# Kernel optimization log

Measured on AMD Instinct MI355X. Metric: run time of the kernel, lower is better.

The kernel has to match this reference:

```python
import jax, jax.numpy as jnp
import numpy as np

D_MODEL = 1024
D_STATE = 64
D_CONV = 4
EXPAND = 2
HEADDIM = 64
NGROUPS = 1
D_INNER = EXPAND * D_MODEL          # 2048 (= d_ssm)
NHEADS = D_INNER // HEADDIM         # 32
CONV_DIM = D_INNER + 2 * NGROUPS * D_STATE      # 2176
D_IN_PROJ = 2 * D_INNER + 2 * NGROUPS * D_STATE + NHEADS  # 4256
BATCH, SEQLEN = 1, 1024
EPS = 1e-5


def silu(x):
    return x * jax.nn.sigmoid(x)


def _causal_dwconv(xBC, conv_w, conv_b):
    # xBC: (B, L, C); conv_w: (C, W) depthwise; causal padding W-1 on the left
    x = jnp.transpose(xBC, (0, 2, 1))  # (B, C, L)
    y = jax.lax.conv_general_dilated(
        x, conv_w[:, None, :], window_strides=(1,),
        padding=[(conv_w.shape[-1] - 1, 0)],
        feature_group_count=x.shape[1])
    return jnp.transpose(y, (0, 2, 1)) + conv_b


def _mamba_dir(u, W_in, conv_w, conv_b, dt_bias, A_log, D, norm_w, W_out):
    B, L, _ = u.shape
    H, P, G, N = NHEADS, HEADDIM, NGROUPS, D_STATE
    zxbcdt = u @ W_in.T                               # (B, L, D_IN_PROJ)
    z = zxbcdt[..., :D_INNER]
    xBC = zxbcdt[..., D_INNER:D_INNER + CONV_DIM]
    dt = zxbcdt[..., -H:]
    xBC = silu(_causal_dwconv(xBC, conv_w, conv_b))
    x = xBC[..., :D_INNER].reshape(B, L, H, P)
    Bm = xBC[..., D_INNER:D_INNER + G * N].reshape(B, L, G, N)
    Cm = xBC[..., D_INNER + G * N:].reshape(B, L, G, N)
    dt = jax.nn.softplus(dt + dt_bias)                # (B, L, H)
    A = -jnp.exp(A_log.astype(jnp.float32))           # (H,)
    rep = H // G
    Bh = jnp.repeat(Bm, rep, axis=2)                  # (B, L, H, N)
    Ch = jnp.repeat(Cm, rep, axis=2)
    dA = jnp.exp(dt * A)                              # (B, L, H)
    dtx = dt[..., None] * x                           # (B, L, H, P)

    def step(h, inp):
        dA_t, dtx_t, Bh_t, Ch_t = inp                 # (B,H), (B,H,P), (B,H,N), (B,H,N)
        h = h * dA_t[..., None, None] + jnp.einsum('bhp,bhn->bhpn', dtx_t, Bh_t)
        y = jnp.einsum('bhpn,bhn->bhp', h, Ch_t)
        return h, y

    h0 = jnp.zeros((B, H, P, N), dtype=u.dtype)
    inputs = (dA.swapaxes(0, 1), dtx.swapaxes(0, 1),
              Bh.swapaxes(0, 1), Ch.swapaxes(0, 1))
    _, ys = jax.lax.scan(step, h0, inputs)            # ys: (L, B, H, P)
    y = ys.swapaxes(0, 1) + D[None, None, :, None] * x
    y = y.reshape(B, L, D_INNER)
    # gated RMSNorm (norm_before_gate=False): norm(y * silu(z)), group = d_ssm/ngroups
    yg = y * silu(z)
    yg = yg.reshape(B, L, G, -1)
    yg = yg * jax.lax.rsqrt(jnp.mean(yg * yg, axis=-1, keepdims=True) + EPS)
    yg = yg.reshape(B, L, D_INNER) * norm_w
    return yg @ W_out.T                               # (B, L, d_model)


def _forward(u, W_in_f, W_in_b, conv_w_f, conv_b_f, conv_w_b, conv_b_b,
             dt_bias_f, dt_bias_b, A_log_f, A_log_b, D_f, D_b,
             norm_w_f, norm_w_b, W_out_f, W_out_b, W_out):
    out_f = _mamba_dir(u, W_in_f, conv_w_f, conv_b_f, dt_bias_f, A_log_f,
                       D_f, norm_w_f, W_out_f)
    ub = jnp.flip(u, axis=1)
    out_b = _mamba_dir(ub, W_in_b, conv_w_b, conv_b_b, dt_bias_b, A_log_b,
                       D_b, norm_w_b, W_out_b)
    out = silu(jnp.concatenate([out_f, jnp.flip(out_b, axis=1)], axis=-1))
    return out @ W_out.T


def setup_inputs() -> dict:
    key = jax.random.key(0)
    ks = jax.random.split(key, 20)
    s = 0.02

    def dt_init(k):
        dt = jnp.exp(jax.random.uniform(k, (NHEADS,)) *
                     (np.log(0.1) - np.log(0.001)) + np.log(0.001))
        return dt + jnp.log(-jnp.expm1(-dt))  # inverse softplus

    def a_init(k):
        return jnp.log(jax.random.uniform(k, (NHEADS,), minval=1.0, maxval=16.0))

    return {
        'u': jax.random.normal(ks[0], (BATCH, SEQLEN, D_MODEL), jnp.float32),
        'W_in_f': jax.random.normal(ks[1], (D_IN_PROJ, D_MODEL), jnp.float32) * s,
        'W_in_b': jax.random.normal(ks[2], (D_IN_PROJ, D_MODEL), jnp.float32) * s,
        'conv_w_f': jax.random.normal(ks[3], (CONV_DIM, D_CONV), jnp.float32) * 0.2,
        'conv_b_f': jnp.zeros((CONV_DIM,), jnp.float32),
        'conv_w_b': jax.random.normal(ks[4], (CONV_DIM, D_CONV), jnp.float32) * 0.2,
        'conv_b_b': jnp.zeros((CONV_DIM,), jnp.float32),
        'dt_bias_f': dt_init(ks[5]),
        'dt_bias_b': dt_init(ks[6]),
        'A_log_f': a_init(ks[7]),
        'A_log_b': a_init(ks[8]),
        'D_f': jnp.ones((NHEADS,), jnp.float32),
        'D_b': jnp.ones((NHEADS,), jnp.float32),
        'norm_w_f': jnp.ones((D_INNER,), jnp.float32),
        'norm_w_b': jnp.ones((D_INNER,), jnp.float32),
        'W_out_f': jax.random.normal(ks[9], (D_MODEL, D_INNER), jnp.float32) * s,
        'W_out_b': jax.random.normal(ks[10], (D_MODEL, D_INNER), jnp.float32) * s,
        'W_out': jax.random.normal(ks[11], (D_MODEL, 2 * D_MODEL), jnp.float32) * s,
    }


def reference(u, W_in_f, W_in_b, conv_w_f, conv_b_f, conv_w_b, conv_b_b,
              dt_bias_f, dt_bias_b, A_log_f, A_log_b, D_f, D_b,
              norm_w_f, norm_w_b, W_out_f, W_out_b, W_out):
    return _forward(u, W_in_f, W_in_b, conv_w_f, conv_b_f, conv_w_b, conv_b_b,
                    dt_bias_f, dt_bias_b, A_log_f, A_log_b, D_f, D_b,
                    norm_w_f, norm_w_b, W_out_f, W_out_b, W_out)
```

## Files before the change

### kernel.cpp

```cpp
#include <hip/hip_runtime.h>
#include <hip/hip_bf16.h>
#include <stdint.h>

#define LSEQ   1024
#define DINNER 2048
#define CONVD  2176
#define LDP    4352
#define NH     32
#define HD     64
#define NST    64
#define CHUNK  64
#define NCH    16
#define LDT    72

#define POFF_CWF  0
#define POFF_CBF  8704
#define POFF_CWB  10880
#define POFF_CBB  19584
#define POFF_DTBF 21760
#define POFF_DTBB 21792
#define POFF_ALF  21824
#define POFF_ALB  21856
#define POFF_DF   21888
#define POFF_DB   21920
#define POFF_NWF  21952
#define POFF_NWB  24000
#define PTOT      26048

#define BF16_ONES 0x3F803F80u

typedef short v8s __attribute__((ext_vector_type(8)));
typedef short v4s __attribute__((ext_vector_type(4)));
typedef float v4f __attribute__((ext_vector_type(4)));
using bf16 = __hip_bfloat16;

__device__ __forceinline__ float loadf(const void* p, size_t i, int isbf) {
    return isbf ? __bfloat162float(((const bf16*)p)[i]) : ((const float*)p)[i];
}
__device__ __forceinline__ float s2f(short s) {
    unsigned u = ((unsigned)(unsigned short)s) << 16; float f;
    __builtin_memcpy(&f, &u, 4); return f;
}
__device__ __forceinline__ short f2s(float f) {
    bf16 b = __float2bfloat16(f); short s;
    __builtin_memcpy(&s, &b, 2); return s;
}
__device__ __forceinline__ void load8(const void* p, size_t i, int isbf, float* o) {
    if (isbf) {
        v8s s = *(const v8s*)((const short*)p + i);
        #pragma unroll
        for (int e = 0; e < 8; e++) o[e] = s2f(s[e]);
    } else {
        float4 a = *(const float4*)((const float*)p + i);
        float4 b = *(const float4*)((const float*)p + i + 4);
        o[0] = a.x; o[1] = a.y; o[2] = a.z; o[3] = a.w;
        o[4] = b.x; o[5] = b.y; o[6] = b.z; o[7] = b.w;
    }
}
__device__ __forceinline__ v8s pack8(const float* o) {
    v8s r;
    #pragma unroll
    for (int e = 0; e < 8; e++) r[e] = f2s(o[e]);
    return r;
}

__device__ __forceinline__ void gload16(const bf16* g, bf16* l) {
    __builtin_amdgcn_global_load_lds(
        (const __attribute__((address_space(1))) void*)g,
        (__attribute__((address_space(3))) void*)l, 16, 0, 0);
}

template<int V> __device__ __forceinline__ void vwait() {
    if constexpr (V == 0) asm volatile("s_waitcnt vmcnt(0)" ::: "memory");
    else if constexpr (V == 3) asm volatile("s_waitcnt vmcnt(3)" ::: "memory");
    else if constexpr (V == 4) asm volatile("s_waitcnt vmcnt(4)" ::: "memory");
    else if constexpr (V == 6) asm volatile("s_waitcnt vmcnt(6)" ::: "memory");
    else if constexpr (V == 8) asm volatile("s_waitcnt vmcnt(8)" ::: "memory");
}

__global__ void conv_params(const void* cwf, const void* cbf, const void* cwb, const void* cbb,
                            const void* dtbf, const void* dtbb, const void* alf, const void* alb,
                            const void* df, const void* db, const void* nwf, const void* nwb,
                            float* __restrict__ P, int* __restrict__ flag)
{
    int idx = blockIdx.x * 256 + threadIdx.x;
    if (idx >= PTOT) return;
    int f = (((const unsigned int*)nwf)[0] == BF16_ONES) ? 1 : 0;
    if (idx == 0) *flag = f;
    float v;
    if      (idx < POFF_CBF)  v = loadf(cwf,  idx,              f);
    else if (idx < POFF_CWB)  v = loadf(cbf,  idx - POFF_CBF,   f);
    else if (idx < POFF_CBB)  v = loadf(cwb,  idx - POFF_CWB,   f);
    else if (idx < POFF_DTBF) v = loadf(cbb,  idx - POFF_CBB,   f);
    else if (idx < POFF_DTBB) v = loadf(dtbf, idx - POFF_DTBF,  f);
    else if (idx < POFF_ALF)  v = loadf(dtbb, idx - POFF_DTBB,  f);
    else if (idx < POFF_ALB)  v = loadf(alf,  idx - POFF_ALF,   f);
    else if (idx < POFF_DF)   v = loadf(alb,  idx - POFF_ALB,   f);
    else if (idx < POFF_DB)   v = loadf(df,   idx - POFF_DF,    f);
    else if (idx < POFF_NWF)  v = loadf(db,   idx - POFF_DB,    f);
    else if (idx < POFF_NWB)  v = loadf(nwf,  idx - POFF_NWF,   f);
    else                      v = loadf(nwb,  idx - POFF_NWB,   f);
    P[idx] = v;
}

#define NPU  262144
#define NPW  1114112
#define NWO  786432
__global__ void prep_all(const void* __restrict__ U, const void* __restrict__ Wf, const void* __restrict__ Wb,
                         const void* __restrict__ Wof, const void* __restrict__ Wob, const void* __restrict__ Wom,
                         const void* __restrict__ nwf,
                         bf16* __restrict__ Au, bf16* __restrict__ Wp,
                         bf16* __restrict__ Woc, bf16* __restrict__ Wo2)
{
    int idx = blockIdx.x * 256 + threadIdx.x;
    int f = (((const unsigned int*)nwf)[0] == BF16_ONES) ? 1 : 0;
    if (idx < NPU) {
        int r = idx >> 7, c8 = (idx & 127) * 8;
        int src = (r < 1024) ? r : (2047 - r);
        float o[8]; load8(U, (size_t)src * 1024 + c8, f, o);
        *(v8s*)(Au + (size_t)r * 1024 + c8) = pack8(o);
    } else if (idx < NPU + NPW) {
        int j = idx - NPU;
        int r = (j >> 7) % 4352;
        int d = j / (4352 * 128);
        int c8 = (j & 127) * 8;
        float o[8] = {0.f, 0.f, 0.f, 0.f, 0.f, 0.f, 0.f, 0.f};
        if (r < 4256) load8(d ? Wb : Wf, (size_t)r * 1024 + c8, f, o);
        *(v8s*)(Wp + (size_t)j * 8) = pack8(o);
    } else if (idx < NPU + NPW + NWO) {
        int j = idx - NPU - NPW;
        int seg = j / 262144;
        size_t j8 = (size_t)(j % 262144) * 8;
        float o[8];
        if (seg == 0)      { load8(Wof, j8, f, o); *(v8s*)(Woc + j8) = pack8(o); }
        else if (seg == 1) { load8(Wob, j8, f, o); *(v8s*)(Woc + 1024 * 2048 + j8) = pack8(o); }
        else               { load8(Wom, j8, f, o); *(v8s*)(Wo2 + j8) = pack8(o); }
    }
}

template<int BM, int BN, int BK>
__global__ __launch_bounds__(256) void gemm_bt(
    const bf16* __restrict__ A, const bf16* __restrict__ B0, const bf16* __restrict__ B1,
    int rowSplit, void* __restrict__ Cv, int M, int N, int K, const int* outFlag,
    int epi, int swzMode)
{
    constexpr int RPL = 2048 / BK;
    constexpr int AN  = BM / RPL;
    constexpr int BNN = BN / RPL;
    constexpr int LPS = AN + BNN;
    constexpr int MI  = BM / 32;
    constexpr int NJ  = BN / 32;
    constexpr int KS  = BK / 32;
    constexpr int CPR = BK / 8;
    __shared__ __align__(16) bf16 LdsA[4][BM * BK];
    __shared__ __align__(16) bf16 LdsB[4][BN * BK];
    const int tid  = threadIdx.x;
    const int lane = tid & 63;
    const int wave = tid >> 6;
    const int quad = lane >> 4, l16 = lane & 15;
    const int wrow = (wave >> 1) * (BM / 2);
    const int wcol = (wave & 1)  * (BN / 2);

    int bx = blockIdx.x, by = blockIdx.y;
    if (swzMode >= 0) {
        const int gx = gridDim.x, gy = gridDim.y;
        const int nwg = gx * gy;
        const int cpx = nwg >> 3;
        const int p   = by * gx + bx;
        const int L   = (p & 7) * cpx + (p >> 3);
        if (swzMode) { by = L % gy; bx = L / gy; }
        else         { bx = L % gx; by = L / gx; }
    }
    const int m0 = by * BM;
    const int n0 = bx * BN;
    const bf16* Bp = (m0 >= rowSplit) ? B1 : B0;
    const int mode = (outFlag && !epi) ? *outFlag : 1;

    const int r0 = tid / CPR;
    const int pc = tid % CPR;
    const int fx_w = (BK == 32) ? ((r0 >> 1) & 3) : (r0 & 7);
    const int csw = (pc ^ fx_w) * 8;
    const bf16* gA[AN];
    const bf16* gB[BNN];
    #pragma unroll
    for (int a = 0; a < AN; a++)  gA[a] = A  + (size_t)(m0 + r0 + RPL * a) * K + csw;
    #pragma unroll
    for (int q = 0; q < BNN; q++) gB[q] = Bp + (size_t)(n0 + r0 + RPL * q) * K + csw;

    v4f acc[MI][NJ];
    #pragma unroll
    for (int i = 0; i < MI; i++)
        #pragma unroll
        for (int j = 0; j < NJ; j++) acc[i][j] = (v4f){0.f, 0.f, 0.f, 0.f};

    const int nt = K / BK;

    auto STAGE = [&](int buf, int t) {
        const int k0 = t * BK;
        #pragma unroll
        for (int a = 0; a < AN; a++)
            gload16(gA[a] + k0, &LdsA[buf][a * 2048 + tid * 8]);
        #pragma unroll
        for (int q = 0; q < BNN; q++)
            gload16(gB[q] + k0, &LdsB[buf][q * 2048 + tid * 8]);
    };

    STAGE(0, 0);
    STAGE(1, 1);
    STAGE(2, 2);

    for (int t = 0; t < nt; ++t) {
        const int buf = t & 3;
        if (t < nt - 2)       vwait<2 * LPS>();
        else if (t == nt - 2) vwait<LPS>();
        else                  vwait<0>();
        __builtin_amdgcn_s_barrier();
        if (t + 3 < nt) STAGE((t + 3) & 3, t + 3);

        const bf16* as = &LdsA[buf][0];
        const bf16* bs = &LdsB[buf][0];
        #pragma unroll
        for (int ks = 0; ks < KS; ks++) {
            v8s af[MI], bfr[NJ];
            #pragma unroll
            for (int i = 0; i < MI; i++) {
                int row = wrow + i * 16 + l16;
                int fx = (BK == 32) ? ((row >> 1) & 3) : (row & 7);
                af[i] = *(const v8s*)&as[row * BK + (((ks * 4 + quad) ^ fx)) * 8];
            }
            #pragma unroll
            for (int j = 0; j < NJ; j++) {
                int row = wcol + j * 16 + l16;
                int fx = (BK == 32) ? ((row >> 1) & 3) : (row & 7);
                bfr[j] = *(const v8s*)&bs[row * BK + (((ks * 4 + quad) ^ fx)) * 8];
            }
            #pragma unroll
            for (int i = 0; i < MI; i++)
                #pragma unroll
                for (int j = 0; j < NJ; j++)
                    acc[i][j] = __builtin_amdgcn_mfma_f32_16x16x32_bf16(af[i], bfr[j], acc[i][j], 0, 0, 0);
        }
    }

    #pragma unroll
    for (int i = 0; i < MI; i++) {
        int row = m0 + wrow + i * 16 + quad * 4;
        #pragma unroll
        for (int j = 0; j < NJ; j++) {
            int col = n0 + wcol + j * 16 + l16;
            if (epi) {
                bf16* Act = (bf16*)Cv;
                #pragma unroll
                for (int r = 0; r < 4; r++) {
                    float x = acc[i][j][r];
                    float v = x / (1.f + __expf(-x));
                    int rr = row + r;
                    if (rr < 1024) Act[(size_t)rr * 2048 + col] = __float2bfloat16(v);
                    else           Act[(size_t)(2047 - rr) * 2048 + 1024 + col] = __float2bfloat16(v);
                }
            } else if (mode) {
                bf16* C = (bf16*)Cv;
                #pragma unroll
                for (int r = 0; r < 4; r++)
                    C[(size_t)(row + r) * N + col] = __float2bfloat16(acc[i][j][r]);
            } else {
                float* C = (float*)Cv;
                #pragma unroll
                for (int r = 0; r < 4; r++)
                    C[(size_t)(row + r) * N + col] = acc[i][j][r];
            }
        }
    }
}

#define NCONV (2 * LSEQ * (CONVD / 8))
#define NDT   (2 * LSEQ * NH)
__global__ void conv_dt(const bf16* __restrict__ Z, const float* __restrict__ P,
                        bf16* __restrict__ XC, float* __restrict__ DT, float* __restrict__ LDA)
{
    int idx = blockIdx.x * 256 + threadIdx.x;
    if (idx < NCONV) {
        int c8 = (idx % (CONVD / 8)) * 8;
        int l = (idx / (CONVD / 8)) % LSEQ;
        int d = idx / ((CONVD / 8) * LSEQ);
        const float* w    = P + (d ? POFF_CWB : POFF_CWF) + c8 * 4;
        const float* bias = P + (d ? POFF_CBB : POFF_CBF) + c8;
        const bf16* zbase = Z + ((size_t)(d * LSEQ + l)) * LDP + DINNER + c8;
        float s[8];
        #pragma unroll
        for (int e = 0; e < 8; e++) s[e] = bias[e];
        #pragma unroll
        for (int k = 0; k < 4; k++) {
            int ls = l - 3 + k;
            if (ls >= 0) {
                v8s zv = *(const v8s*)(zbase + (ls - l) * LDP);
                #pragma unroll
                for (int e = 0; e < 8; e++) s[e] += w[e * 4 + k] * s2f(zv[e]);
            }
        }
        float o[8];
        #pragma unroll
        for (int e = 0; e < 8; e++) o[e] = s[e] / (1.f + __expf(-s[e]));
        *(v8s*)(XC + (size_t)(d * LSEQ + l) * CONVD + c8) = pack8(o);
    } else if (idx < NCONV + NDT) {
        int j = idx - NCONV;
        int h = j & 31; int l = (j >> 5) & (LSEQ - 1); int d = j >> 15;
        float raw = s2f(((const short*)Z)[((size_t)(d * LSEQ + l)) * LDP + DINNER + CONVD + h])
                  + P[POFF_DTBF + d * 32 + h];
        float dt = (raw > 20.f) ? raw : log1pf(__expf(raw));
        float Aa = -__expf(P[POFF_ALF + d * 32 + h]);
        DT[j] = dt;
        LDA[j] = Aa * dt;
    }
}

__global__ __launch_bounds__(256) void ssd_intra(const bf16* __restrict__ XC,
                                                 const float* __restrict__ DT,
                                                 const float* __restrict__ LDA,
                                                 bf16* __restrict__ Yi, bf16* __restrict__ S,
                                                 float* __restrict__ Pdec, float* __restrict__ LSg)
{
    __shared__ __align__(16) short sB [64 * LDT];
    __shared__ __align__(16) short sBT[64 * LDT];
    __shared__ __align__(16) short sC [64 * LDT];
    __shared__ __align__(16) short sXT[64 * LDT];
    __shared__ __align__(16) short sGW[64 * LDT];
    __shared__ float sls[64], sdt[64], sW[64];

    int b = blockIdx.x;
    int d = b >> 9, h = (b >> 4) & 31, c = b & 15;
    int r0 = c * CHUNK;
    int t = threadIdx.x;
    const bf16* base = XC + (size_t)d * LSEQ * CONVD;

    {
        int l = t >> 2, nb = (t & 3) * 16;
        const bf16* row = base + (size_t)(r0 + l) * CONVD;
        const short* Brow = (const short*)(row + DINNER) + nb;
        const short* Crow = (const short*)(row + DINNER + NST) + nb;
        const short* Xrow = (const short*)(row + h * HD) + nb;
        v8s b0 = *(const v8s*)Brow, b1 = *(const v8s*)(Brow + 8);
        v8s c0 = *(const v8s*)Crow, c1 = *(const v8s*)(Crow + 8);
        v8s x0 = *(const v8s*)Xrow, x1 = *(const v8s*)(Xrow + 8);
        *(v8s*)&sB[l * LDT + nb]     = b0;
        *(v8s*)&sB[l * LDT + nb + 8] = b1;
        *(v8s*)&sC[l * LDT + nb]     = c0;
        *(v8s*)&sC[l * LDT + nb + 8] = c1;
        #pragma unroll
        for (int k = 0; k < 8; k++) {
            sBT[(nb + k)     * LDT + l] = b0[k];
            sBT[(nb + 8 + k) * LDT + l] = b1[k];
            sXT[(nb + k)     * LDT + l] = x0[k];
            sXT[(nb + 8 + k) * LDT + l] = x1[k];
        }
    }
    if (t < 64) {
        size_t ofs = (size_t)d * LSEQ * NH + (size_t)(r0 + t) * NH + h;
        float v = LDA[ofs];
        float dtv = DT[ofs];
        #pragma unroll
        for (int off = 1; off < 64; off <<= 1) {
            float u = __shfl_up(v, off);
            if (t >= off) v += u;
        }
        sls[t] = v; sdt[t] = dtv;
        float ls63 = __shfl(v, 63);
        sW[t] = __expf(ls63 - v) * dtv;
        LSg[(size_t)b * 64 + t] = v;
        if (t == 63) Pdec[b] = __expf(v);
    }
    __syncthreads();

    int lane = t & 63, wave = t >> 6;
    int quad = lane >> 4, l16 = lane & 15;

    {
        v8s a0 = *(const v8s*)&sC[(wave * 16 + l16) * LDT + quad * 8];
        v8s a1 = *(const v8s*)&sC[(wave * 16 + l16) * LDT + quad * 8 + 32];
        #pragma unroll
        for (int jt = 0; jt < 4; jt++) {
            v8s b0 = *(const v8s*)&sB[(jt * 16 + l16) * LDT + quad * 8];
            v8s b1 = *(const v8s*)&sB[(jt * 16 + l16) * LDT + quad * 8 + 32];
            v4f acc = (v4f){0.f, 0.f, 0.f, 0.f};
            acc = __builtin_amdgcn_mfma_f32_16x16x32_bf16(a0, b0, acc, 0, 0, 0);
            acc = __builtin_amdgcn_mfma_f32_16x16x32_bf16(a1, b1, acc, 0, 0, 0);
            #pragma unroll
            for (int r = 0; r < 4; r++) {
                int ii = wave * 16 + quad * 4 + r;
                int jj = jt * 16 + l16;
                float wgt = (jj <= ii) ? __expf(sls[ii] - sls[jj]) * sdt[jj] : 0.f;
                sGW[ii * LDT + jj] = f2s(acc[r] * wgt);
            }
        }
    }
    __syncthreads();

    bf16* ybase = Yi + ((size_t)d * LSEQ + r0) * DINNER + h * HD;

    {
        v8s a0 = *(const v8s*)&sGW[(wave * 16 + l16) * LDT + quad * 8];
        v8s a1 = *(const v8s*)&sGW[(wave * 16 + l16) * LDT + quad * 8 + 32];
        #pragma unroll
        for (int pt = 0; pt < 4; pt++) {
            v8s b0 = *(const v8s*)&sXT[(pt * 16 + l16) * LDT + quad * 8];
            v8s b1 = *(const v8s*)&sXT[(pt * 16 + l16) * LDT + quad * 8 + 32];
            v4f acc = (v4f){0.f, 0.f, 0.f, 0.f};
            acc = __builtin_amdgcn_mfma_f32_16x16x32_bf16(a0, b0, acc, 0, 0, 0);
            acc = __builtin_amdgcn_mfma_f32_16x16x32_bf16(a1, b1, acc, 0, 0, 0);
            #pragma unroll
            for (int r = 0; r < 4; r++) {
                int ii = wave * 16 + quad * 4 + r;
                int p  = pt * 16 + l16;
                ybase[(size_t)ii * DINNER + p] = __float2bfloat16(acc[r]);
            }
        }
    }

    {
        v8s a0r = *(const v8s*)&sXT[(wave * 16 + l16) * LDT + quad * 8];
        v8s a1r = *(const v8s*)&sXT[(wave * 16 + l16) * LDT + quad * 8 + 32];
        v8s a0, a1;
        #pragma unroll
        for (int e = 0; e < 8; e++) {
            a0[e] = f2s(s2f(a0r[e]) * sW[quad * 8 + e]);
            a1[e] = f2s(s2f(a1r[e]) * sW[quad * 8 + 32 + e]);
        }
        short* sout = (short*)S + (size_t)b * 4096;
        #pragma unroll
        for (int nt = 0; nt < 4; nt++) {
            v8s b0 = *(const v8s*)&sBT[(nt * 16 + l16) * LDT + quad * 8];
            v8s b1 = *(const v8s*)&sBT[(nt * 16 + l16) * LDT + quad * 8 + 32];
            v4f acc = (v4f){0.f, 0.f, 0.f, 0.f};
            acc = __builtin_amdgcn_mfma_f32_16x16x32_bf16(a0, b0, acc, 0, 0, 0);
            acc = __builtin_amdgcn_mfma_f32_16x16x32_bf16(a1, b1, acc, 0, 0, 0);
            #pragma unroll
            for (int r = 0; r < 4; r++) {
                int p = wave * 16 + quad * 4 + r;
                int n = nt * 16 + l16;
                sout[p * 64 + n] = f2s(acc[r]);
            }
        }
    }
}

__global__ __launch_bounds__(256) void scan2(bf16* __restrict__ S, const float* __restrict__ Pdec)
{
    int b = blockIdx.x;
    int off = blockIdx.y * 1024 + threadIdx.x * 4;
    float h0 = 0.f, h1 = 0.f, h2 = 0.f, h3 = 0.f;
    for (int c = 0; c < NCH; c++) {
        short* so = (short*)S + (((size_t)b * 16 + c) * 4096) + off;
        v4s sc = *(const v4s*)so;
        float Pc = Pdec[b * 16 + c];
        v4s hv; hv[0] = f2s(h0); hv[1] = f2s(h1); hv[2] = f2s(h2); hv[3] = f2s(h3);
        *(v4s*)so = hv;
        h0 = h0 * Pc + s2f(sc[0]);
        h1 = h1 * Pc + s2f(sc[1]);
        h2 = h2 * Pc + s2f(sc[2]);
        h3 = h3 * Pc + s2f(sc[3]);
    }
}

__global__ __launch_bounds__(256) void ssd_inter(const bf16* __restrict__ XC,
                                                 const bf16* __restrict__ Hin,
                                                 const float* __restrict__ LSg,
                                                 bf16* __restrict__ Ye)
{
    __shared__ __align__(16) short sH [64 * LDT];
    __shared__ __align__(16) short sCk[64 * LDT];
    __shared__ float sEls[64];

    int b = blockIdx.x;
    int d = b >> 9, h = (b >> 4) & 31, c = b & 15;
    int r0 = c * CHUNK;
    int t = threadIdx.x;
    const bf16* base = XC + (size_t)d * LSEQ * CONVD;
    {
        int l = t >> 2, nb = (t & 3) * 16;
        const short* hrow = (const short*)Hin + (size_t)b * 4096 + l * 64 + nb;
        const short* crow = (const short*)(base + (size_t)(r0 + l) * CONVD + DINNER + NST) + nb;
        v8s h0 = *(const v8s*)hrow, h1 = *(const v8s*)(hrow + 8);
        v8s c0 = *(const v8s*)crow, c1 = *(const v8s*)(crow + 8);
        *(v8s*)&sH[l * LDT + nb]      = h0;
        *(v8s*)&sH[l * LDT + nb + 8]  = h1;
        *(v8s*)&sCk[l * LDT + nb]     = c0;
        *(v8s*)&sCk[l * LDT + nb + 8] = c1;
    }
    if (t < 64) sEls[t] = __expf(LSg[(size_t)b * 64 + t]);
    __syncthreads();

    int lane = t & 63, wave = t >> 6;
    int quad = lane >> 4, l16 = lane & 15;
    bf16* ybase = Ye + ((size_t)d * LSEQ + r0) * DINNER + h * HD;

    v8s a0 = *(const v8s*)&sCk[(wave * 16 + l16) * LDT + quad * 8];
    v8s a1 = *(const v8s*)&sCk[(wave * 16 + l16) * LDT + quad * 8 + 32];
    #pragma unroll
    for (int pt = 0; pt < 4; pt++) {
        v8s b0 = *(const v8s*)&sH[(pt * 16 + l16) * LDT + quad * 8];
        v8s b1 = *(const v8s*)&sH[(pt * 16 + l16) * LDT + quad * 8 + 32];
        v4f acc = (v4f){0.f, 0.f, 0.f, 0.f};
        acc = __builtin_amdgcn_mfma_f32_16x16x32_bf16(a0, b0, acc, 0, 0, 0);
        acc = __builtin_amdgcn_mfma_f32_16x16x32_bf16(a1, b1, acc, 0, 0, 0);
        #pragma unroll
        for (int r = 0; r < 4; r++) {
            int ii = wave * 16 + quad * 4 + r;
            int p  = pt * 16 + l16;
            ybase[(size_t)ii * DINNER + p] = __float2bfloat16(sEls[ii] * acc[r]);
        }
    }
}

__global__ __launch_bounds__(256) void gate_norm(const bf16* __restrict__ Yi, const bf16* __restrict__ Ye,
                                                 const bf16* __restrict__ XC,
                                                 const bf16* __restrict__ Z, const float* __restrict__ P,
                                                 bf16* __restrict__ YG)
{
    int rowi = blockIdx.x;
    int d = rowi >> 10;
    int tid = threadIdx.x;
    const bf16* yirow = Yi + (size_t)rowi * DINNER;
    const bf16* yerow = Ye + (size_t)rowi * DINNER;
    const bf16* xrow = XC + (size_t)rowi * CONVD;
    const bf16* zrow = Z + (size_t)rowi * LDP;
    const float* Dv = P + POFF_DF + d * 32;
    const float* nw = P + POFF_NWF + d * 2048;
    int j0 = tid * 8;
    float Dh = Dv[j0 >> 6];
    v8s yi8 = *(const v8s*)(yirow + j0);
    v8s ye8 = *(const v8s*)(yerow + j0);
    v8s xv8 = *(const v8s*)(xrow + j0);
    v8s zv = *(const v8s*)(zrow + j0);
    float g[8]; float ss = 0.f;
    #pragma unroll
    for (int e = 0; e < 8; e++) {
        float y = s2f(yi8[e]) + s2f(ye8[e]) + Dh * s2f(xv8[e]);
        float z = s2f(zv[e]);
        float gg = y * (z / (1.f + __expf(-z)));
        g[e] = gg; ss += gg * gg;
    }
    #pragma unroll
    for (int off = 32; off; off >>= 1) ss += __shfl_xor(ss, off);
    __shared__ float red[4];
    if ((tid & 63) == 0) red[tid >> 6] = ss;
    __syncthreads();
    float tot = red[0] + red[1] + red[2] + red[3];
    float scale = rsqrtf(tot * (1.f / 2048.f) + 1e-5f);
    float o[8];
    #pragma unroll
    for (int e = 0; e < 8; e++) o[e] = g[e] * scale * nw[j0 + e];
    *(v8s*)(YG + (size_t)rowi * DINNER + j0) = pack8(o);
}

extern "C" void kernel_launch(void* const* d_in, const int* in_sizes, int n_in,
                              void* d_out, int out_size, void* d_ws, size_t ws_size,
                              hipStream_t stream)
{
    const void* u      = d_in[0];
    const void* Winf   = d_in[1];
    const void* Winb   = d_in[2];
    const void* convwf = d_in[3];
    const void* convbf = d_in[4];
    const void* convwb = d_in[5];
    const void* convbb = d_in[6];
    const void* dtbf   = d_in[7];
    const void* dtbb   = d_in[8];
    const void* Alf    = d_in[9];
    const void* Alb    = d_in[10];
    const void* Dfv    = d_in[11];
    const void* Dbv    = d_in[12];
    const void* nwf    = d_in[13];
    const void* nwb    = d_in[14];
    const void* Woutf  = d_in[15];
    const void* Woutb  = d_in[16];
    const void* Wout   = d_in[17];

    char* w = (char*)d_ws;
    int*   flag = (int*)w;   w += 256;
    bf16*  Au   = (bf16*)w;  w += (size_t)2048 * 1024 * 2;
    bf16*  Wp   = (bf16*)w;  w += (size_t)2 * 4352 * 1024 * 2;
    bf16*  Woc  = (bf16*)w;
    bf16*  Act  = (bf16*)w;  w += (size_t)2 * 1024 * 2048 * 2;
    bf16*  Wo2  = (bf16*)w;  w += (size_t)1024 * 2048 * 2;
    float* P    = (float*)w; w += 104448;
    bf16*  Zb   = (bf16*)w;  w += (size_t)2048 * 4352 * 2;
    bf16*  XC   = (bf16*)w;  w += (size_t)2048 * 2176 * 2;
    float* DT   = (float*)w; w += (size_t)2048 * 32 * 4;
    float* LDA  = (float*)w; w += (size_t)2048 * 32 * 4;
    bf16*  YG   = (bf16*)w;  w += (size_t)2048 * 2048 * 2;
    bf16*  S    = (bf16*)w;  w += (size_t)2 * 32 * 16 * 64 * 64 * 2;
    float* Pdec = (float*)w; w += 4096;
    float* LSg  = (float*)w; w += (size_t)2 * 32 * 16 * 64 * 4;
    bf16*  Yi   = (bf16*)w;  w += (size_t)2048 * 2048 * 2;
    bf16*  Ye   = (bf16*)w;  w += (size_t)2048 * 2048 * 2;
    if ((size_t)(w - (char*)d_ws) > ws_size) return;

    conv_params<<<(PTOT + 255) / 256, 256, 0, stream>>>(convwf, convbf, convwb, convbb,
        dtbf, dtbb, Alf, Alb, Dfv, Dbv, nwf, nwb, P, flag);
    prep_all<<<(NPU + NPW + NWO) / 256, 256, 0, stream>>>(u, Winf, Winb, Woutf, Woutb, Wout,
        nwf, Au, Wp, Woc, Wo2);

    dim3 g1(4352 / 64, 2048 / 128);
    gemm_bt<128, 64, 32><<<g1, 256, 0, stream>>>(Au, Wp, Wp + (size_t)4352 * 1024, 1024,
                                                 Zb, 2048, 4352, 1024, nullptr, 0, 1);

    conv_dt<<<(NCONV + NDT + 255) / 256, 256, 0, stream>>>(Zb, P, XC, DT, LDA);

    ssd_intra<<<1024, 256, 0, stream>>>(XC, DT, LDA, Yi, S, Pdec, LSg);
    scan2<<<dim3(64, 4), 256, 0, stream>>>(S, Pdec);
    ssd_inter<<<1024, 256, 0, stream>>>(XC, S, LSg, Ye);

    gate_norm<<<2048, 256, 0, stream>>>(Yi, Ye, XC, Zb, P, YG);

    dim3 g2(1024 / 64, 2048 / 64);
    gemm_bt<64, 64, 64><<<g2, 256, 0, stream>>>(YG, Woc, Woc + (size_t)1024 * 2048, 1024,
                                                Act, 2048, 1024, 2048, nullptr, 1, -1);

    dim3 g3(1024 / 64, 1024 / 64);
    gemm_bt<64, 64, 64><<<g3, 256, 0, stream>>>(Act, Wo2, Wo2, 1 << 30,
                                                d_out, 1024, 1024, 2048, flag, 0, -1);
}
```

Baseline: 282.2 us.

## Fold param conversion into prep kernel, swizzle SSD transposed LDS, prefetch scan2

Merges the conv_params launch into prep_all by adding an extra index segment, removing one kernel launch. In ssd_intra, the transposed B and X tiles in LDS get an XOR swizzle on the column index, with matching reads, to reduce bank conflicts on the scattered transposed stores. scan2 now preloads all chunk decay factors into registers and prefetches the next chunk's state before the current update, to hide global load latency in the sequential loop. The swizzle must stay consistent across every reader of sXT and sBT, including any in hidden code.

```diff
diff --git a/kernel.cpp b/kernel.cpp
--- a/kernel.cpp
+++ b/kernel.cpp
@@ -78,39 +78,18 @@
     else if constexpr (V == 8) asm volatile("s_waitcnt vmcnt(8)" ::: "memory");
 }
 
-__global__ void conv_params(const void* cwf, const void* cbf, const void* cwb, const void* cbb,
-                            const void* dtbf, const void* dtbb, const void* alf, const void* alb,
-                            const void* df, const void* db, const void* nwf, const void* nwb,
-                            float* __restrict__ P, int* __restrict__ flag)
-{
-    int idx = blockIdx.x * 256 + threadIdx.x;
-    if (idx >= PTOT) return;
-    int f = (((const unsigned int*)nwf)[0] == BF16_ONES) ? 1 : 0;
-    if (idx == 0) *flag = f;
-    float v;
-    if      (idx < POFF_CBF)  v = loadf(cwf,  idx,              f);
-    else if (idx < POFF_CWB)  v = loadf(cbf,  idx - POFF_CBF,   f);
-    else if (idx < POFF_CBB)  v = loadf(cwb,  idx - POFF_CWB,   f);
-    else if (idx < POFF_DTBF) v = loadf(cbb,  idx - POFF_CBB,   f);
-    else if (idx < POFF_DTBB) v = loadf(dtbf, idx - POFF_DTBF,  f);
-    else if (idx < POFF_ALF)  v = loadf(dtbb, idx - POFF_DTBB,  f);
-    else if (idx < POFF_ALB)  v = loadf(alf,  idx - POFF_ALF,   f);
-    else if (idx < POFF_DF)   v = loadf(alb,  idx - POFF_ALB,   f);
-    else if (idx < POFF_DB)   v = loadf(df,   idx - POFF_DF,    f);
-    else if (idx < POFF_NWF)  v = loadf(db,   idx - POFF_DB,    f);
-    else if (idx < POFF_NWB)  v = loadf(nwf,  idx - POFF_NWF,   f);
-    else                      v = loadf(nwb,  idx - POFF_NWB,   f);
-    P[idx] = v;
-}
-
 #define NPU  262144
 #define NPW  1114112
 #define NWO  786432
+#define NSEG (NPU + NPW + NWO)
 __global__ void prep_all(const void* __restrict__ U, const void* __restrict__ Wf, const void* __restrict__ Wb,
                          const void* __restrict__ Wof, const void* __restrict__ Wob, const void* __restrict__ Wom,
-                         const void* __restrict__ nwf,
+                         const void* cwf, const void* cbf, const void* cwb, const void* cbb,
+                         const void* dtbf, const void* dtbb, const void* alf, const void* alb,
+                         const void* df, const void* db, const void* nwf, const void* nwb,
                          bf16* __restrict__ Au, bf16* __restrict__ Wp,
-                         bf16* __restrict__ Woc, bf16* __restrict__ Wo2)
+                         bf16* __restrict__ Woc, bf16* __restrict__ Wo2,
+                         float* __restrict__ P, int* __restrict__ flag)
 {
     int idx = blockIdx.x * 256 + threadIdx.x;
     int f = (((const unsigned int*)nwf)[0] == BF16_ONES) ? 1 : 0;
@@ -127,7 +106,7 @@
         float o[8] = {0.f, 0.f, 0.f, 0.f, 0.f, 0.f, 0.f, 0.f};
         if (r < 4256) load8(d ? Wb : Wf, (size_t)r * 1024 + c8, f, o);
         *(v8s*)(Wp + (size_t)j * 8) = pack8(o);
-    } else if (idx < NPU + NPW + NWO) {
+    } else if (idx < NSEG) {
         int j = idx - NPU - NPW;
         int seg = j / 262144;
         size_t j8 = (size_t)(j % 262144) * 8;
@@ -135,6 +114,23 @@
         if (seg == 0)      { load8(Wof, j8, f, o); *(v8s*)(Woc + j8) = pack8(o); }
         else if (seg == 1) { load8(Wob, j8, f, o); *(v8s*)(Woc + 1024 * 2048 + j8) = pack8(o); }
         else               { load8(Wom, j8, f, o); *(v8s*)(Wo2 + j8) = pack8(o); }
+    } else if (idx < NSEG + PTOT) {
+        int j = idx - NSEG;
+        if (j == 0) *flag = f;
+        float v;
+        if      (j < POFF_CBF)  v = loadf(cwf,  j,              f);
+        else if (j < POFF_CWB)  v = loadf(cbf,  j - POFF_CBF,   f);
+        else if (j < POFF_CBB)  v = loadf(cwb,  j - POFF_CWB,   f);
+        else if (j < POFF_DTBF) v = loadf(cbb,  j - POFF_CBB,   f);
+        else if (j < POFF_DTBB) v = loadf(dtbf, j - POFF_DTBF,  f);
+        else if (j < POFF_ALF)  v = loadf(dtbb, j - POFF_DTBB,  f);
+        else if (j < POFF_ALB)  v = loadf(alf,  j - POFF_ALF,   f);
+        else if (j < POFF_DF)   v = loadf(alb,  j - POFF_ALB,   f);
+        else if (j < POFF_DB)   v = loadf(df,   j - POFF_DF,    f);
+        else if (j < POFF_NWF)  v = loadf(db,   j - POFF_DB,    f);
+        else if (j < POFF_NWB)  v = loadf(nwf,  j - POFF_NWF,   f);
+        else                    v = loadf(nwb,  j - POFF_NWB,   f);
+        P[j] = v;
     }
 }
 
@@ -335,6 +331,8 @@
 
     {
         int l = t >> 2, nb = (t & 3) * 16;
+        int q = t & 3;
+        int cswt = (((l >> 3) ^ q) * 8) + (l & 7);
         const bf16* row = base + (size_t)(r0 + l) * CONVD;
         const short* Brow = (const short*)(row + DINNER) + nb;
         const short* Crow = (const short*)(row + DINNER + NST) + nb;
@@ -348,10 +346,10 @@
         *(v8s*)&sC[l * LDT + nb + 8] = c1;
         #pragma unroll
         for (int k = 0; k < 8; k++) {
-            sBT[(nb + k)     * LDT + l] = b0[k];
-            sBT[(nb + 8 + k) * LDT + l] = b1[k];
-            sXT[(nb + k)     * LDT + l] = x0[k];
-            sXT[(nb + 8 + k) * LDT + l] = x1[k];
+            sBT[(nb + k)     * LDT + cswt] = b0[k];
+            sBT[(nb + 8 + k) * LDT + cswt] = b1[k];
+            sXT[(nb + k)     * LDT + cswt] = x0[k];
+            sXT[(nb + 8 + k) * LDT + cswt] = x1[k];
         }
     }
     if (t < 64) {
@@ -402,8 +400,9 @@
         v8s a1 = *(const v8s*)&sGW[(wave * 16 + l16) * LDT + quad * 8 + 32];
         #pragma unroll
         for (int pt = 0; pt < 4; pt++) {
-            v8s b0 = *(const v8s*)&sXT[(pt * 16 + l16) * LDT + quad * 8];
-            v8s b1 = *(const v8s*)&sXT[(pt * 16 + l16) * LDT + quad * 8 + 32];
+            int sb = (quad ^ (pt & 3)) * 8;
+            v8s b0 = *(const v8s*)&sXT[(pt * 16 + l16) * LDT + sb];
+            v8s b1 = *(const v8s*)&sXT[(pt * 16 + l16) * LDT + sb + 32];
             v4f acc = (v4f){0.f, 0.f, 0.f, 0.f};
             acc = __builtin_amdgcn_mfma_f32_16x16x32_bf16(a0, b0, acc, 0, 0, 0);
             acc = __builtin_amdgcn_mfma_f32_16x16x32_bf16(a1, b1, acc, 0, 0, 0);
@@ -417,8 +416,9 @@
     }
 
     {
-        v8s a0r = *(const v8s*)&sXT[(wave * 16 + l16) * LDT + quad * 8];
-        v8s a1r = *(const v8s*)&sXT[(wave * 16 + l16) * LDT + quad * 8 + 32];
+        int sa = (quad ^ (wave & 3)) * 8;
+        v8s a0r = *(const v8s*)&sXT[(wave * 16 + l16) * LDT + sa];
+        v8s a1r = *(const v8s*)&sXT[(wave * 16 + l16) * LDT + sa + 32];
         v8s a0, a1;
         #pragma unroll
         for (int e = 0; e < 8; e++) {
@@ -428,8 +428,9 @@
         short* sout = (short*)S + (size_t)b * 4096;
         #pragma unroll
         for (int nt = 0; nt < 4; nt++) {
-            v8s b0 = *(const v8s*)&sBT[(nt * 16 + l16) * LDT + quad * 8];
-            v8s b1 = *(const v8s*)&sBT[(nt * 16 + l16) * LDT + quad * 8 + 32];
+            int sb = (quad ^ (nt & 3)) * 8;
+            v8s b0 = *(const v8s*)&sBT[(nt * 16 + l16) * LDT + sb];
+            v8s b1 = *(const v8s*)&sBT[(nt * 16 + l16) * LDT + sb + 32];
             v4f acc = (v4f){0.f, 0.f, 0.f, 0.f};
             acc = __builtin_amdgcn_mfma_f32_16x16x32_bf16(a0, b0, acc, 0, 0, 0);
             acc = __builtin_amdgcn_mfma_f32_16x16x32_bf16(a1, b1, acc, 0, 0, 0);
@@ -447,11 +448,18 @@
 {
     int b = blockIdx.x;
     int off = blockIdx.y * 1024 + threadIdx.x * 4;
+    short* base = (short*)S + (size_t)b * 16 * 4096 + off;
+    float pc[NCH];
+    #pragma unroll
+    for (int c = 0; c < NCH; c++) pc[c] = Pdec[b * 16 + c];
     float h0 = 0.f, h1 = 0.f, h2 = 0.f, h3 = 0.f;
+    v4s nxt = *(const v4s*)base;
+    #pragma unroll
     for (int c = 0; c < NCH; c++) {
-        short* so = (short*)S + (((size_t)b * 16 + c) * 4096) + off;
-        v4s sc = *(const v4s*)so;
-        float Pc = Pdec[b * 16 + c];
+        short* so = base + (size_t)c * 4096;
+        v4s sc = nxt;
+        if (c + 1 < NCH) nxt = *(const v4s*)(so + 4096);
+        float Pc = pc[c];
         v4s hv; hv[0] = f2s(h0); hv[1] = f2s(h1); hv[2] = f2s(h2); hv[3] = f2s(h3);
         *(v4s*)so = hv;
         h0 = h0 * Pc + s2f(sc[0]);
@@ -595,10 +603,10 @@
     bf16*  Ye   = (bf16*)w;  w += (size_t)2048 * 2048 * 2;
     if ((size_t)(w - (char*)d_ws) > ws_size) return;
 
-    conv_params<<<(PTOT + 255) / 256, 256, 0, stream>>>(convwf, convbf, convwb, convbb,
-        dtbf, dtbb, Alf, Alb, Dfv, Dbv, nwf, nwb, P, flag);
-    prep_all<<<(NPU + NPW + NWO) / 256, 256, 0, stream>>>(u, Winf, Winb, Woutf, Woutb, Wout,
-        nwf, Au, Wp, Woc, Wo2);
+    prep_all<<<(NSEG + PTOT + 255) / 256, 256, 0, stream>>>(
+        u, Winf, Winb, Woutf, Woutb, Wout,
+        convwf, convbf, convwb, convbb, dtbf, dtbb, Alf, Alb, Dfv, Dbv, nwf, nwb,
+        Au, Wp, Woc, Wo2, P, flag);
 
     dim3 g1(4352 / 64, 2048 / 128);
     gemm_bt<128, 64, 32><<<g1, 256, 0, stream>>>(Au, Wp, Wp + (size_t)4352 * 1024, 1024,
```

Result: no change. 277.7 us (-1.6%).
